# Optimization experiments

Hardware: AMD Instinct MI355X
Metric: run time of the kernel (lower is better)

The kernel has to match this reference:

```python
import jax, jax.numpy as jnp
import numpy as np

NUM_HEADS = 8
ALPHA = 4.0  # spikingjelly sigmoid surrogate default

@jax.custom_vjp
def spike(x):
    return (x >= 0.0).astype(x.dtype)

def _spike_fwd(x):
    return spike(x), x

def _spike_bwd(x, g):
    s = jax.nn.sigmoid(ALPHA * x)
    return (g * ALPHA * s * (1.0 - s),)

spike.defvjp(_spike_fwd, _spike_bwd)

def lif(x, v_th=1.0, tau=2.0):
    # multi-step LIF over leading T dim; v_reset=0, hard reset, detach_reset
    def step(v, xt):
        h = v + (xt - v) / tau
        s = spike(h - v_th)
        v_new = h * (1.0 - jax.lax.stop_gradient(s))
        return v_new, s
    _, out = jax.lax.scan(step, jnp.zeros_like(x[0]), x)
    return out

def bn(x, gamma, beta, mean, var, eps=1e-5):
    # inference BatchNorm2d on (N,C,H,W)
    inv = gamma / jnp.sqrt(var + eps)
    return x * inv[None, :, None, None] + (beta - mean * inv)[None, :, None, None]

def conv1x1(x, w, b=None):
    # x: (N,C,H,W), w: (O,C)
    y = jnp.einsum('nchw,oc->nohw', x, w)
    if b is not None:
        y = y + b[None, :, None, None]
    return y

def setup_inputs() -> dict:
    key = jax.random.key(0)
    ks = jax.random.split(key, 20)
    T, B, C, H, W = 4, 32, 384, 14, 14
    d = {
        'x': jax.random.normal(ks[0], (T, B, C, H, W), jnp.float32),
        'q_w': jax.random.normal(ks[1], (C, C), jnp.float32) * (1.0 / np.sqrt(C)),
        'q_gamma': jax.random.uniform(ks[2], (C,), jnp.float32),
        'q_beta': jax.random.normal(ks[3], (C,), jnp.float32) * 0.1,
        'q_mean': jax.random.normal(ks[4], (C,), jnp.float32) * 0.1,
        'q_var': jax.random.uniform(ks[5], (C,), jnp.float32) + 0.5,
        'k_w': jax.random.normal(ks[6], (C, C), jnp.float32) * (1.0 / np.sqrt(C)),
        'k_gamma': jax.random.uniform(ks[7], (C,), jnp.float32),
        'k_beta': jax.random.normal(ks[8], (C,), jnp.float32) * 0.1,
        'k_mean': jax.random.normal(ks[9], (C,), jnp.float32) * 0.1,
        'k_var': jax.random.uniform(ks[10], (C,), jnp.float32) + 0.5,
        'proj_w': jax.random.normal(ks[11], (C, C), jnp.float32) * (1.0 / np.sqrt(C)),
        'proj_b': jax.random.normal(ks[12], (C,), jnp.float32) * 0.1,
        'proj_gamma': jax.random.uniform(ks[13], (C,), jnp.float32),
        'proj_beta': jax.random.normal(ks[14], (C,), jnp.float32) * 0.1,
        'proj_mean': jax.random.normal(ks[15], (C,), jnp.float32) * 0.1,
        'proj_var': jax.random.uniform(ks[16], (C,), jnp.float32) + 0.5,
    }
    return d

def reference(x, q_w, q_gamma, q_beta, q_mean, q_var,
              k_w, k_gamma, k_beta, k_mean, k_var,
              proj_w, proj_b, proj_gamma, proj_beta, proj_mean, proj_var):
    T, B, C, H, W = x.shape
    dh = C // NUM_HEADS
    xf = x.reshape(T * B, C, H, W)
    # Q branch: conv1x1 -> BN -> multistep LIF
    q = bn(conv1x1(xf, q_w), q_gamma, q_beta, q_mean, q_var).reshape(T, B, C, H, W)
    q = lif(q).reshape(T, B, NUM_HEADS, dh, H, W)
    # K branch
    k = bn(conv1x1(xf, k_w), k_gamma, k_beta, k_mean, k_var).reshape(T, B, C, H, W)
    k = lif(k).reshape(T, B, NUM_HEADS, dh, H, W)
    # sum-pool attention: sum q over head feature dim, spike it, gate k
    qs = jnp.sum(q, axis=3, keepdims=True)          # (T,B,heads,1,H,W)
    attn = lif(qs, v_th=0.5)
    y = (attn * k).reshape(T * B, C, H, W)
    # output projection: conv1x1(+bias) -> BN -> LIF
    y = bn(conv1x1(y, proj_w, proj_b), proj_gamma, proj_beta, proj_mean, proj_var)
    y = lif(y.reshape(T, B, C, H, W))
    return y
```

## Files before the change

kernel.cpp:

```cpp
#include <hip/hip_runtime.h>

#define C_DIM 384
#define S_DIM 196
#define CS_   (C_DIM * S_DIM)
#define BCS   (32 * CS_)
#define NELEM (128 * CS_)
#define NBS   6272

typedef _Float16 half8  __attribute__((ext_vector_type(8)));
typedef float    floatx4 __attribute__((ext_vector_type(4)));

__device__ __forceinline__ void gl_lds16(const _Float16* g, _Float16* l) {
    __builtin_amdgcn_global_load_lds(
        (const __attribute__((address_space(1))) unsigned int*)g,
        (__attribute__((address_space(3))) unsigned int*)l, 16, 0, 0);
}

__global__ __launch_bounds__(256)
void split_w(const float* __restrict__ qw, const float* __restrict__ kw,
             const float* __restrict__ pw,
             const float* qg, const float* qb, const float* qm, const float* qv,
             const float* kg, const float* kb, const float* km, const float* kv,
             const float* pg, const float* pb, const float* pm, const float* pv,
             _Float16* __restrict__ Wq0, _Float16* __restrict__ Wq1,
             _Float16* __restrict__ Wp0, _Float16* __restrict__ Wp1,
             float2* __restrict__ invshQ, float2* __restrict__ invshP)
{
    const int i = blockIdx.x * 256 + threadIdx.x;
    const int NQ = 768 * C_DIM;
    if (i < NQ) {
        const int o = i / C_DIM, c = i - o * C_DIM;
        const float v = (o < 384) ? qw[o * C_DIM + c] : kw[(o - 384) * C_DIM + c];
        const _Float16 h0 = (_Float16)v;
        Wq0[i] = h0;
        Wq1[i] = (_Float16)((v - (float)h0) * 4096.0f);
    } else if (i < NQ + C_DIM * C_DIM) {
        const int j = i - NQ;
        const float v = pw[j];
        const _Float16 h0 = (_Float16)v;
        Wp0[j] = h0;
        Wp1[j] = (_Float16)((v - (float)h0) * 4096.0f);
    }
    if (i < 768) {
        float g, b, m, vv;
        if (i < 384) { g = qg[i]; b = qb[i]; m = qm[i]; vv = qv[i]; }
        else         { g = kg[i-384]; b = kb[i-384]; m = km[i-384]; vv = kv[i-384]; }
        const float inv = g / sqrtf(vv + 1e-5f);
        invshQ[i] = make_float2(inv, b - m * inv);
    } else if (i < 1152) {
        const int j = i - 768;
        const float inv = pg[j] / sqrtf(pv[j] + 1e-5f);
        invshP[j] = make_float2(inv, pb[j] - pm[j] * inv);
    }
}

__global__ __launch_bounds__(256)
void split_x(const float* __restrict__ X,
             _Float16* __restrict__ X0, _Float16* __restrict__ X1)
{
    __shared__ float tile[32][201];
    const int tb = blockIdx.x;
    const int tt = tb >> 5, b = tb & 31;
    const int c0 = blockIdx.y * 32;
    const int t  = threadIdx.x;
    for (int idx = t; idx < 32 * S_DIM; idx += 256) {
        const int cc = idx / S_DIM, s = idx - cc * S_DIM;
        tile[cc][s] = X[(size_t)tb * CS_ + (c0 + cc) * S_DIM + s];
    }
    __syncthreads();
    for (int idx = t; idx < 32 * S_DIM; idx += 256) {
        const int s = idx >> 5, cc = idx & 31;
        const float v = tile[cc][s];
        const _Float16 h0 = (_Float16)v;
        const size_t off = ((size_t)(b * S_DIM + s) * 4 + tt) * C_DIM + c0 + cc;
        X0[off] = h0;
        X1[off] = (_Float16)((v - (float)h0) * 4096.0f);
    }
}

__global__ __launch_bounds__(256, 3)
void qk_mfma(const _Float16* __restrict__ A0, const _Float16* __restrict__ A1,
             const _Float16* __restrict__ B0, const _Float16* __restrict__ B1,
             const float2* __restrict__ invsh,
             unsigned char* __restrict__ spkQ, unsigned char* __restrict__ spkK)
{
    __shared__ __align__(16) _Float16 As0[128 * 32];
    __shared__ __align__(16) _Float16 As1[128 * 32];
    __shared__ __align__(16) _Float16 Bs0[128 * 32];
    __shared__ __align__(16) _Float16 Bs1[128 * 32];

    const int t    = threadIdx.x;
    const int wave = t >> 6, lane = t & 63;
    const int m0 = blockIdx.x * 128;
    const int o0 = blockIdx.y * 128;

    const int wR   = wave * 32;
    const int sRow = lane >> 2;
    const int sCol = (((lane & 3) ^ ((sRow >> 1) & 3))) << 3;

    const int lo = lane & 15, quad = lane >> 4;
    const int oq = (wave >> 1) * 64, mq = (wave & 1) * 64;
    const int rdC = (quad ^ ((lo >> 1) & 3)) << 3;

    floatx4 acc[4][4];
    #pragma unroll
    for (int i = 0; i < 4; ++i)
        #pragma unroll
        for (int j = 0; j < 4; ++j) acc[i][j] = (floatx4)0.0f;

    for (int kt = 0; kt < 12; ++kt) {
        __syncthreads();
        const int kb = kt * 32;
        #pragma unroll
        for (int u = 0; u < 2; ++u) {
            const int R = wR + u * 16;
            const size_t ga = (size_t)(o0 + R + sRow) * C_DIM + kb + sCol;
            const size_t gb = (size_t)(m0 + R + sRow) * C_DIM + kb + sCol;
            gl_lds16(A0 + ga, &As0[R * 32]);
            gl_lds16(A1 + ga, &As1[R * 32]);
            gl_lds16(B0 + gb, &Bs0[R * 32]);
            gl_lds16(B1 + gb, &Bs1[R * 32]);
        }
        __syncthreads();

        half8 w0F[4], w1F[4], x0F[4], x1F[4];
        #pragma unroll
        for (int j = 0; j < 4; ++j) {
            const int ra = (oq + j * 16 + lo) * 32 + rdC;
            w0F[j] = *(const half8*)&As0[ra];
            w1F[j] = *(const half8*)&As1[ra];
        }
        #pragma unroll
        for (int i = 0; i < 4; ++i) {
            const int rb = (mq + i * 16 + lo) * 32 + rdC;
            x0F[i] = *(const half8*)&Bs0[rb];
            x1F[i] = *(const half8*)&Bs1[rb];
        }
        #pragma unroll
        for (int i = 0; i < 4; ++i) {
            const half8 xS = x0F[i] * (_Float16)4096.0f;
            #pragma unroll
            for (int j = 0; j < 4; ++j) {
                acc[i][j] = __builtin_amdgcn_mfma_f32_16x16x32_f16(
                    x0F[i], w1F[j], acc[i][j], 0, 0, 0);
                acc[i][j] = __builtin_amdgcn_mfma_f32_16x16x32_f16(
                    x1F[i], w0F[j], acc[i][j], 0, 0, 0);
                acc[i][j] = __builtin_amdgcn_mfma_f32_16x16x32_f16(
                    xS,     w0F[j], acc[i][j], 0, 0, 0);
            }
        }
    }

    #pragma unroll
    for (int j = 0; j < 4; ++j) {
        const int o = o0 + oq + j * 16 + lo;
        const float2 is = invsh[o];
        const float inv = is.x * (1.0f / 4096.0f);
        const float sh  = is.y;
        unsigned char* base = (o < 384) ? spkQ : spkK;
        const int orow = (o < 384) ? o : o - 384;
        #pragma unroll
        for (int i = 0; i < 4; ++i) {
            const int bs = ((m0 + mq + i * 16) >> 2) + quad;
            float v = 0.0f; int bits = 0;
            #pragma unroll
            for (int r = 0; r < 4; ++r) {
                const float xv = acc[i][j][r] * inv + sh;
                const float h = v + (xv - v) * 0.5f;
                const int sp = (h >= 1.0f);
                v = sp ? 0.0f : h;
                bits |= sp << r;
            }
            base[(size_t)bs * C_DIM + orow] = (unsigned char)bits;
        }
    }
}

__global__ __launch_bounds__(256)
void attn_compute(const unsigned char* __restrict__ spkQ,
                  unsigned char* __restrict__ attnB)
{
    const int idx = blockIdx.x * 256 + threadIdx.x;
    if (idx >= NBS * 8) return;
    const int bs = idx >> 3, head = idx & 7;
    const unsigned long long* p =
        (const unsigned long long*)(spkQ + (size_t)bs * C_DIM + head * 48);
    int qs[4] = {0, 0, 0, 0};
    #pragma unroll
    for (int u = 0; u < 6; ++u) {
        const unsigned long long v = p[u];
        qs[0] += __popcll(v & 0x0101010101010101ull);
        qs[1] += __popcll(v & 0x0202020202020202ull);
        qs[2] += __popcll(v & 0x0404040404040404ull);
        qs[3] += __popcll(v & 0x0808080808080808ull);
    }
    float va = 0.0f;
    int bits = 0;
    #pragma unroll
    for (int t = 0; t < 4; ++t) {
        const float h = va + ((float)qs[t] - va) * 0.5f;
        const int a = (h >= 0.5f);
        va = a ? 0.0f : h;
        bits |= a << t;
    }
    attnB[idx] = (unsigned char)bits;
}

__global__ __launch_bounds__(256, 3)
void proj_mfma(const _Float16* __restrict__ A0, const _Float16* __restrict__ A1,
               const unsigned char* __restrict__ spkK,
               const unsigned char* __restrict__ attnB,
               const float* __restrict__ bias, const float2* __restrict__ invsh,
               float* __restrict__ out)
{
    __shared__ __align__(16) _Float16 smem[3 * 128 * 32];
    _Float16* As0 = smem;
    _Float16* As1 = smem + 4096;
    _Float16* Bs0 = smem + 8192;

    const int t    = threadIdx.x;
    const int wave = t >> 6, lane = t & 63;
    const int m0 = blockIdx.x * 128;
    const int o0 = blockIdx.y * 128;

    const int wR   = wave * 32;
    const int sRow = lane >> 2;
    const int sCol = (((lane & 3) ^ ((sRow >> 1) & 3))) << 3;
    const int gC8  = (lane & 3) << 3;
    const int pC8  = sCol;

    const int lo = lane & 15, quad = lane >> 4;
    const int oq = (wave >> 1) * 64, mq = (wave & 1) * 64;
    const int rdC = (quad ^ ((lo >> 1) & 3)) << 3;

    const int bsL[2] = { (m0 + wR +  0 + sRow) >> 2, (m0 + wR + 16 + sRow) >> 2 };
    const int ttL    = (m0 + wR + sRow) & 3;

    floatx4 acc[4][4];
    #pragma unroll
    for (int i = 0; i < 4; ++i)
        #pragma unroll
        for (int j = 0; j < 4; ++j) acc[i][j] = (floatx4)0.0f;

    unsigned long long rk[2];
    int rab[2];
    {
        const int head0 = gC8 / 48;
        #pragma unroll
        for (int u = 0; u < 2; ++u) {
            rk[u]  = *(const unsigned long long*)(spkK + (size_t)bsL[u] * C_DIM + gC8);
            rab[u] = (attnB[bsL[u] * 8 + head0] >> ttL) & 1;
        }
    }

    for (int kt = 0; kt < 12; ++kt) {
        __syncthreads();
        const int kb = kt * 32;
        #pragma unroll
        for (int u = 0; u < 2; ++u) {
            const int R = wR + u * 16;
            half8 bv;
            #pragma unroll
            for (int e = 0; e < 8; ++e)
                bv[e] = (_Float16)(float)((int)(rk[u] >> (8 * e + ttL)) & rab[u] & 1);
            *(half8*)&Bs0[(R + sRow) * 32 + pC8] = bv;
            const size_t ga = (size_t)(o0 + R + sRow) * C_DIM + kb + sCol;
            gl_lds16(A0 + ga, &As0[R * 32]);
            gl_lds16(A1 + ga, &As1[R * 32]);
        }
        if (kt < 11) {
            const int kb2  = (kt + 1) * 32;
            const int head = (kb2 + gC8) / 48;
            #pragma unroll
            for (int u = 0; u < 2; ++u) {
                rk[u]  = *(const unsigned long long*)(spkK + (size_t)bsL[u] * C_DIM + kb2 + gC8);
                rab[u] = (attnB[bsL[u] * 8 + head] >> ttL) & 1;
            }
        }
        __syncthreads();

        half8 w0F[4], w1F[4], yF[4];
        #pragma unroll
        for (int j = 0; j < 4; ++j) {
            const int ra = (oq + j * 16 + lo) * 32 + rdC;
            w0F[j] = *(const half8*)&As0[ra];
            w1F[j] = *(const half8*)&As1[ra];
        }
        #pragma unroll
        for (int i = 0; i < 4; ++i)
            yF[i] = *(const half8*)&Bs0[(mq + i * 16 + lo) * 32 + rdC];

        #pragma unroll
        for (int j = 0; j < 4; ++j) {
            const half8 wS = w0F[j] * (_Float16)4096.0f;
            #pragma unroll
            for (int i = 0; i < 4; ++i) {
                acc[i][j] = __builtin_amdgcn_mfma_f32_16x16x32_f16(
                    yF[i], w1F[j], acc[i][j], 0, 0, 0);
                acc[i][j] = __builtin_amdgcn_mfma_f32_16x16x32_f16(
                    yF[i], wS,     acc[i][j], 0, 0, 0);
            }
        }
    }

    int bits[4][4];
    #pragma unroll
    for (int j = 0; j < 4; ++j) {
        const int o = o0 + oq + j * 16 + lo;
        const float2 is = invsh[o];
        const float bv = bias[o];
        #pragma unroll
        for (int i = 0; i < 4; ++i) {
            float v = 0.0f; int bt = 0;
            #pragma unroll
            for (int r = 0; r < 4; ++r) {
                const float p = acc[i][j][r] * (1.0f / 4096.0f);
                const float z = (p + bv) * is.x + is.y;
                const float h = v + (z - v) * 0.5f;
                const int sp = (h >= 1.0f);
                v = sp ? 0.0f : h;
                bt |= sp << r;
            }
            bits[i][j] = bt;
        }
    }

    float* tile = (float*)smem;
    const int bs0g = m0 >> 2;
    for (int r = 0; r < 4; ++r) {
        __syncthreads();
        #pragma unroll
        for (int j = 0; j < 4; ++j)
            #pragma unroll
            for (int i = 0; i < 4; ++i)
                tile[(oq + j * 16 + lo) * 33 + (mq >> 2) + i * 4 + quad] =
                    ((bits[i][j] >> r) & 1) ? 1.0f : 0.0f;
        __syncthreads();
        #pragma unroll
        for (int it = 0; it < 4; ++it) {
            const int idx = it * 256 + t;
            const int o   = idx >> 3;
            const int ch  = idx & 7;
            const int bsg = bs0g + ch * 4;
            const int b   = bsg / S_DIM;
            const int s   = bsg - b * S_DIM;
            float4 vv;
            vv.x = tile[o * 33 + ch * 4 + 0];
            vv.y = tile[o * 33 + ch * 4 + 1];
            vv.z = tile[o * 33 + ch * 4 + 2];
            vv.w = tile[o * 33 + ch * 4 + 3];
            *(float4*)(out + (size_t)r * BCS + (size_t)b * CS_
                           + (size_t)(o0 + o) * S_DIM + s) = vv;
        }
    }
}

extern "C" void kernel_launch(void* const* d_in, const int* in_sizes, int n_in,
                              void* d_out, int out_size, void* d_ws, size_t ws_size,
                              hipStream_t stream)
{
    const float* x          = (const float*)d_in[0];
    const float* q_w        = (const float*)d_in[1];
    const float* q_gamma    = (const float*)d_in[2];
    const float* q_beta     = (const float*)d_in[3];
    const float* q_mean     = (const float*)d_in[4];
    const float* q_var      = (const float*)d_in[5];
    const float* k_w        = (const float*)d_in[6];
    const float* k_gamma    = (const float*)d_in[7];
    const float* k_beta     = (const float*)d_in[8];
    const float* k_mean     = (const float*)d_in[9];
    const float* k_var      = (const float*)d_in[10];
    const float* proj_w     = (const float*)d_in[11];
    const float* proj_b     = (const float*)d_in[12];
    const float* proj_gamma = (const float*)d_in[13];
    const float* proj_beta  = (const float*)d_in[14];
    const float* proj_mean  = (const float*)d_in[15];
    const float* proj_var   = (const float*)d_in[16];
    float* out = (float*)d_out;

    _Float16* h0 = (_Float16*)d_ws;
    _Float16* h1 = h0 + NELEM;
    _Float16* Wq0 = h1 + NELEM;
    _Float16* Wq1 = Wq0 + 768 * C_DIM;
    _Float16* Wp0 = Wq1 + 768 * C_DIM;
    _Float16* Wp1 = Wp0 + C_DIM * C_DIM;
    float2*   invshQ = (float2*)(Wp1 + C_DIM * C_DIM);
    float2*   invshP = invshQ + 768;
    unsigned char* spkQ  = (unsigned char*)(invshP + 384);
    unsigned char* spkK  = spkQ + (size_t)NBS * C_DIM;
    unsigned char* attnB = spkK + (size_t)NBS * C_DIM;

    split_w<<<1728, 256, 0, stream>>>(q_w, k_w, proj_w,
                                      q_gamma, q_beta, q_mean, q_var,
                                      k_gamma, k_beta, k_mean, k_var,
                                      proj_gamma, proj_beta, proj_mean, proj_var,
                                      Wq0, Wq1, Wp0, Wp1, invshQ, invshP);
    split_x<<<dim3(128, 12), 256, 0, stream>>>(x, h0, h1);

    qk_mfma<<<dim3(196, 6), 256, 0, stream>>>(Wq0, Wq1, h0, h1, invshQ,
                                              spkQ, spkK);
    attn_compute<<<196, 256, 0, stream>>>(spkQ, attnB);
    proj_mfma<<<dim3(196, 3), 256, 0, stream>>>(Wp0, Wp1, spkK, attnB,
                                                proj_b, invshP, out);
}
```

Before: 204.5 us.

## Merge prep kernels, fuse attention into projection, swap grid axes

Combines the weight-split and input-split kernels into one launch, and computes the attention spikes inside proj_mfma from spkQ into shared memory, which removes the attn_compute kernel and its global round trip. The grid axes of both GEMM kernels are swapped so that adjacent blocks share the same activation rows across output tiles, which should improve L2 reuse. Each of the three proj blocks that cover the same rows now recomputes the same attention bytes, and the merged prep kernel declares a shared tile that its weight branch does not use.

```diff
diff --git a/kernel.cpp b/kernel.cpp
--- a/kernel.cpp
+++ b/kernel.cpp
@@ -17,64 +17,64 @@
 }
 
 __global__ __launch_bounds__(256)
-void split_w(const float* __restrict__ qw, const float* __restrict__ kw,
-             const float* __restrict__ pw,
-             const float* qg, const float* qb, const float* qm, const float* qv,
-             const float* kg, const float* kb, const float* km, const float* kv,
-             const float* pg, const float* pb, const float* pm, const float* pv,
-             _Float16* __restrict__ Wq0, _Float16* __restrict__ Wq1,
-             _Float16* __restrict__ Wp0, _Float16* __restrict__ Wp1,
-             float2* __restrict__ invshQ, float2* __restrict__ invshP)
-{
-    const int i = blockIdx.x * 256 + threadIdx.x;
-    const int NQ = 768 * C_DIM;
-    if (i < NQ) {
-        const int o = i / C_DIM, c = i - o * C_DIM;
-        const float v = (o < 384) ? qw[o * C_DIM + c] : kw[(o - 384) * C_DIM + c];
-        const _Float16 h0 = (_Float16)v;
-        Wq0[i] = h0;
-        Wq1[i] = (_Float16)((v - (float)h0) * 4096.0f);
-    } else if (i < NQ + C_DIM * C_DIM) {
-        const int j = i - NQ;
-        const float v = pw[j];
-        const _Float16 h0 = (_Float16)v;
-        Wp0[j] = h0;
-        Wp1[j] = (_Float16)((v - (float)h0) * 4096.0f);
-    }
-    if (i < 768) {
-        float g, b, m, vv;
-        if (i < 384) { g = qg[i]; b = qb[i]; m = qm[i]; vv = qv[i]; }
-        else         { g = kg[i-384]; b = kb[i-384]; m = km[i-384]; vv = kv[i-384]; }
-        const float inv = g / sqrtf(vv + 1e-5f);
-        invshQ[i] = make_float2(inv, b - m * inv);
-    } else if (i < 1152) {
-        const int j = i - 768;
-        const float inv = pg[j] / sqrtf(pv[j] + 1e-5f);
-        invshP[j] = make_float2(inv, pb[j] - pm[j] * inv);
-    }
-}
-
-__global__ __launch_bounds__(256)
-void split_x(const float* __restrict__ X,
-             _Float16* __restrict__ X0, _Float16* __restrict__ X1)
+void prep(const float* __restrict__ X,
+          const float* __restrict__ qw, const float* __restrict__ kw,
+          const float* __restrict__ pw,
+          const float* qg, const float* qb, const float* qm, const float* qv,
+          const float* kg, const float* kb, const float* km, const float* kv,
+          const float* pg, const float* pb, const float* pm, const float* pv,
+          _Float16* __restrict__ X0, _Float16* __restrict__ X1,
+          _Float16* __restrict__ Wq0, _Float16* __restrict__ Wq1,
+          _Float16* __restrict__ Wp0, _Float16* __restrict__ Wp1,
+          float2* __restrict__ invshQ, float2* __restrict__ invshP)
 {
     __shared__ float tile[32][201];
-    const int tb = blockIdx.x;
-    const int tt = tb >> 5, b = tb & 31;
-    const int c0 = blockIdx.y * 32;
-    const int t  = threadIdx.x;
-    for (int idx = t; idx < 32 * S_DIM; idx += 256) {
-        const int cc = idx / S_DIM, s = idx - cc * S_DIM;
-        tile[cc][s] = X[(size_t)tb * CS_ + (c0 + cc) * S_DIM + s];
-    }
-    __syncthreads();
-    for (int idx = t; idx < 32 * S_DIM; idx += 256) {
-        const int s = idx >> 5, cc = idx & 31;
-        const float v = tile[cc][s];
-        const _Float16 h0 = (_Float16)v;
-        const size_t off = ((size_t)(b * S_DIM + s) * 4 + tt) * C_DIM + c0 + cc;
-        X0[off] = h0;
-        X1[off] = (_Float16)((v - (float)h0) * 4096.0f);
+    const int bid = blockIdx.x;
+    const int t   = threadIdx.x;
+    if (bid < 1536) {
+        const int tb = bid / 12, cch = bid % 12;
+        const int tt = tb >> 5, b = tb & 31;
+        const int c0 = cch * 32;
+        for (int idx = t; idx < 32 * S_DIM; idx += 256) {
+            const int cc = idx / S_DIM, s = idx - cc * S_DIM;
+            tile[cc][s] = X[(size_t)tb * CS_ + (c0 + cc) * S_DIM + s];
+        }
+        __syncthreads();
+        for (int idx = t; idx < 32 * S_DIM; idx += 256) {
+            const int s = idx >> 5, cc = idx & 31;
+            const float v = tile[cc][s];
+            const _Float16 h0 = (_Float16)v;
+            const size_t off = ((size_t)(b * S_DIM + s) * 4 + tt) * C_DIM + c0 + cc;
+            X0[off] = h0;
+            X1[off] = (_Float16)((v - (float)h0) * 4096.0f);
+        }
+    } else {
+        const int i = (bid - 1536) * 256 + t;
+        const int NQ = 768 * C_DIM;
+        if (i < NQ) {
+            const int o = i / C_DIM, c = i - o * C_DIM;
+            const float v = (o < 384) ? qw[o * C_DIM + c] : kw[(o - 384) * C_DIM + c];
+            const _Float16 h0 = (_Float16)v;
+            Wq0[i] = h0;
+            Wq1[i] = (_Float16)((v - (float)h0) * 4096.0f);
+        } else if (i < NQ + C_DIM * C_DIM) {
+            const int j = i - NQ;
+            const float v = pw[j];
+            const _Float16 h0 = (_Float16)v;
+            Wp0[j] = h0;
+            Wp1[j] = (_Float16)((v - (float)h0) * 4096.0f);
+        }
+        if (i < 768) {
+            float g, b2, m, vv;
+            if (i < 384) { g = qg[i]; b2 = qb[i]; m = qm[i]; vv = qv[i]; }
+            else         { g = kg[i-384]; b2 = kb[i-384]; m = km[i-384]; vv = kv[i-384]; }
+            const float inv = g / sqrtf(vv + 1e-5f);
+            invshQ[i] = make_float2(inv, b2 - m * inv);
+        } else if (i < 1152) {
+            const int j = i - 768;
+            const float inv = pg[j] / sqrtf(pv[j] + 1e-5f);
+            invshP[j] = make_float2(inv, pb[j] - pm[j] * inv);
+        }
     }
 }
 
@@ -91,8 +91,8 @@
 
     const int t    = threadIdx.x;
     const int wave = t >> 6, lane = t & 63;
-    const int m0 = blockIdx.x * 128;
-    const int o0 = blockIdx.y * 128;
+    const int o0 = blockIdx.x * 128;
+    const int m0 = blockIdx.y * 128;
 
     const int wR   = wave * 32;
     const int sRow = lane >> 2;
@@ -176,52 +176,23 @@
     }
 }
 
-__global__ __launch_bounds__(256)
-void attn_compute(const unsigned char* __restrict__ spkQ,
-                  unsigned char* __restrict__ attnB)
-{
-    const int idx = blockIdx.x * 256 + threadIdx.x;
-    if (idx >= NBS * 8) return;
-    const int bs = idx >> 3, head = idx & 7;
-    const unsigned long long* p =
-        (const unsigned long long*)(spkQ + (size_t)bs * C_DIM + head * 48);
-    int qs[4] = {0, 0, 0, 0};
-    #pragma unroll
-    for (int u = 0; u < 6; ++u) {
-        const unsigned long long v = p[u];
-        qs[0] += __popcll(v & 0x0101010101010101ull);
-        qs[1] += __popcll(v & 0x0202020202020202ull);
-        qs[2] += __popcll(v & 0x0404040404040404ull);
-        qs[3] += __popcll(v & 0x0808080808080808ull);
-    }
-    float va = 0.0f;
-    int bits = 0;
-    #pragma unroll
-    for (int t = 0; t < 4; ++t) {
-        const float h = va + ((float)qs[t] - va) * 0.5f;
-        const int a = (h >= 0.5f);
-        va = a ? 0.0f : h;
-        bits |= a << t;
-    }
-    attnB[idx] = (unsigned char)bits;
-}
-
 __global__ __launch_bounds__(256, 3)
 void proj_mfma(const _Float16* __restrict__ A0, const _Float16* __restrict__ A1,
+               const unsigned char* __restrict__ spkQ,
                const unsigned char* __restrict__ spkK,
-               const unsigned char* __restrict__ attnB,
                const float* __restrict__ bias, const float2* __restrict__ invsh,
                float* __restrict__ out)
 {
     __shared__ __align__(16) _Float16 smem[3 * 128 * 32];
+    __shared__ unsigned char attnL[256];
     _Float16* As0 = smem;
     _Float16* As1 = smem + 4096;
     _Float16* Bs0 = smem + 8192;
 
     const int t    = threadIdx.x;
     const int wave = t >> 6, lane = t & 63;
-    const int m0 = blockIdx.x * 128;
-    const int o0 = blockIdx.y * 128;
+    const int o0 = blockIdx.x * 128;
+    const int m0 = blockIdx.y * 128;
 
     const int wR   = wave * 32;
     const int sRow = lane >> 2;
@@ -233,8 +204,34 @@
     const int oq = (wave >> 1) * 64, mq = (wave & 1) * 64;
     const int rdC = (quad ^ ((lo >> 1) & 3)) << 3;
 
-    const int bsL[2] = { (m0 + wR +  0 + sRow) >> 2, (m0 + wR + 16 + sRow) >> 2 };
-    const int ttL    = (m0 + wR + sRow) & 3;
+    const int bs0g   = m0 >> 2;
+    const int bsl[2] = { (wR +  0 + sRow) >> 2, (wR + 16 + sRow) >> 2 };
+    const int ttL    = (wR + sRow) & 3;
+
+    {
+        const int bsl_a = t >> 3, head = t & 7;
+        const unsigned long long* p = (const unsigned long long*)
+            (spkQ + (size_t)(bs0g + bsl_a) * C_DIM + head * 48);
+        int qs[4] = {0, 0, 0, 0};
+        #pragma unroll
+        for (int u = 0; u < 6; ++u) {
+            const unsigned long long v = p[u];
+            qs[0] += __popcll(v & 0x0101010101010101ull);
+            qs[1] += __popcll(v & 0x0202020202020202ull);
+            qs[2] += __popcll(v & 0x0404040404040404ull);
+            qs[3] += __popcll(v & 0x0808080808080808ull);
+        }
+        float va = 0.0f; int bits = 0;
+        #pragma unroll
+        for (int tt = 0; tt < 4; ++tt) {
+            const float h = va + ((float)qs[tt] - va) * 0.5f;
+            const int a = (h >= 0.5f);
+            va = a ? 0.0f : h;
+            bits |= a << tt;
+        }
+        attnL[t] = (unsigned char)bits;
+    }
+    __syncthreads();
 
     floatx4 acc[4][4];
     #pragma unroll
@@ -248,8 +245,9 @@
         const int head0 = gC8 / 48;
         #pragma unroll
         for (int u = 0; u < 2; ++u) {
-            rk[u]  = *(const unsigned long long*)(spkK + (size_t)bsL[u] * C_DIM + gC8);
-            rab[u] = (attnB[bsL[u] * 8 + head0] >> ttL) & 1;
+            rk[u]  = *(const unsigned long long*)
+                     (spkK + (size_t)(bs0g + bsl[u]) * C_DIM + gC8);
+            rab[u] = (attnL[bsl[u] * 8 + head0] >> ttL) & 1;
         }
     }
 
@@ -273,8 +271,9 @@
             const int head = (kb2 + gC8) / 48;
             #pragma unroll
             for (int u = 0; u < 2; ++u) {
-                rk[u]  = *(const unsigned long long*)(spkK + (size_t)bsL[u] * C_DIM + kb2 + gC8);
-                rab[u] = (attnB[bsL[u] * 8 + head] >> ttL) & 1;
+                rk[u]  = *(const unsigned long long*)
+                         (spkK + (size_t)(bs0g + bsl[u]) * C_DIM + kb2 + gC8);
+                rab[u] = (attnL[bsl[u] * 8 + head] >> ttL) & 1;
             }
         }
         __syncthreads();
@@ -326,7 +325,6 @@
     }
 
     float* tile = (float*)smem;
-    const int bs0g = m0 >> 2;
     for (int r = 0; r < 4; ++r) {
         __syncthreads();
         #pragma unroll
@@ -388,18 +386,15 @@
     float2*   invshP = invshQ + 768;
     unsigned char* spkQ  = (unsigned char*)(invshP + 384);
     unsigned char* spkK  = spkQ + (size_t)NBS * C_DIM;
-    unsigned char* attnB = spkK + (size_t)NBS * C_DIM;
-
-    split_w<<<1728, 256, 0, stream>>>(q_w, k_w, proj_w,
-                                      q_gamma, q_beta, q_mean, q_var,
-                                      k_gamma, k_beta, k_mean, k_var,
-                                      proj_gamma, proj_beta, proj_mean, proj_var,
-                                      Wq0, Wq1, Wp0, Wp1, invshQ, invshP);
-    split_x<<<dim3(128, 12), 256, 0, stream>>>(x, h0, h1);
-
-    qk_mfma<<<dim3(196, 6), 256, 0, stream>>>(Wq0, Wq1, h0, h1, invshQ,
+
+    prep<<<3264, 256, 0, stream>>>(x, q_w, k_w, proj_w,
+                                   q_gamma, q_beta, q_mean, q_var,
+                                   k_gamma, k_beta, k_mean, k_var,
+                                   proj_gamma, proj_beta, proj_mean, proj_var,
+                                   h0, h1, Wq0, Wq1, Wp0, Wp1, invshQ, invshP);
+
+    qk_mfma<<<dim3(6, 196), 256, 0, stream>>>(Wq0, Wq1, h0, h1, invshQ,
                                               spkQ, spkK);
-    attn_compute<<<196, 256, 0, stream>>>(spkQ, attnB);
-    proj_mfma<<<dim3(196, 3), 256, 0, stream>>>(Wp0, Wp1, spkK, attnB,
+    proj_mfma<<<dim3(3, 196), 256, 0, stream>>>(Wp0, Wp1, spkQ, spkK,
                                                 proj_b, invshP, out);
 }
```

Measured after the change: 205.6 us. No clear change (+0.5%).
